# Optimization experiments

Measured on AMD Instinct MI355X. Metric: run time of the kernel, lower is better.

The kernel has to match this reference:

```python
import jax, jax.numpy as jnp
import numpy as np

HIDDEN_DIM = 256  # scale = sqrt(hidden_dim); D = 2*hidden_dim because is_bi_rnn=True
B, L, D = 4, 4096, 512


def setup_inputs() -> dict:
    key = jax.random.key(0)
    k1, k2, k3, k4, k5 = jax.random.split(key, 5)
    inputs = jax.random.normal(k1, (B, L, D), dtype=jnp.float32)
    # torch nn.Linear(D, D, bias=False) weights, applied as x @ W.T
    Wq = jax.random.normal(k2, (D, D), dtype=jnp.float32) / np.float32(np.sqrt(D))
    Wk = jax.random.normal(k3, (D, D), dtype=jnp.float32) / np.float32(np.sqrt(D))
    Wv = jax.random.normal(k4, (D, D), dtype=jnp.float32) / np.float32(np.sqrt(D))
    # valid lengths per batch element; max must equal L (source uses maxlen = max(lens))
    lens = jax.random.randint(k5, (B,), L // 2, L + 1).at[0].set(L)
    return {"inputs": inputs, "Wq": Wq, "Wk": Wk, "Wv": Wv, "lens": lens}


def reference(inputs, Wq, Wk, Wv, lens):
    # QKV projections (torch Linear: x @ W.T)
    Q = inputs @ Wq.T            # [B, L, D]
    K = inputs @ Wk.T            # [B, L, D]
    V = inputs @ Wv.T            # [B, L, D]
    scale = jnp.asarray(HIDDEN_DIM, inputs.dtype) ** 0.5
    scores = jnp.einsum('bqd,bkd->bqk', Q, K) / scale  # [B, L, L]
    # FAITHFUL: F.softmax with no dim on a 3-D tensor -> legacy torch dim=0 (batch axis)
    W = jax.nn.softmax(scores, axis=0)
    # post-softmax mask over QUERY rows: mask[b, q] = q < lens[b]
    mask = (jnp.arange(L)[None, :] < lens[:, None]).astype(W.dtype)  # [B, L]
    W = W * mask[:, :, None]
    Z = jnp.einsum('bqk,bkd->bqd', W, V)   # [B, L, D]
    return jnp.sum(Z, axis=1, keepdims=True)  # [B, 1, D]
```

## Files before the change

kernel.cpp:

```cpp
#include <hip/hip_runtime.h>

#define BB 4
#define LL 4096
#define DD 512

typedef __attribute__((ext_vector_type(8))) short bf16x8;
typedef __attribute__((ext_vector_type(4))) float f32x4;
typedef __attribute__((ext_vector_type(4))) unsigned short ushort4v;
typedef __attribute__((ext_vector_type(4))) unsigned int u32x4;

__device__ __forceinline__ unsigned short bf16_rne(float x) {
    unsigned u = __float_as_uint(x);
    unsigned r = (u + 0x7FFFu + ((u >> 16) & 1u)) >> 16;
    return (unsigned short)r;
}

__global__ __launch_bounds__(256) void split_x(const float* __restrict__ X,
                                               unsigned short* __restrict__ Xh,
                                               unsigned short* __restrict__ Xl) {
    const size_t i = ((size_t)blockIdx.x * 256 + threadIdx.x) * 4;
    float4 x4 = *reinterpret_cast<const float4*>(X + i);
    float v[4] = {x4.x, x4.y, x4.z, x4.w};
    ushort4v h4, l4;
    #pragma unroll
    for (int j = 0; j < 4; ++j) {
        unsigned short h = bf16_rne(v[j]);
        float lo = v[j] - __uint_as_float((unsigned)h << 16);
        h4[j] = h;
        l4[j] = bf16_rne(lo);
    }
    *reinterpret_cast<ushort4v*>(Xh + i) = h4;
    *reinterpret_cast<ushort4v*>(Xl + i) = l4;
}

__global__ __launch_bounds__(256) void gemm_tn_M(const float* __restrict__ A,
                                                 const float* __restrict__ B,
                                                 unsigned short* __restrict__ Mh,
                                                 unsigned short* __restrict__ Ml,
                                                 float scale) {
    __shared__ float As[16][68];
    __shared__ float Bs[16][68];
    const int tid = threadIdx.x;
    const int tx = tid & 15, ty = tid >> 4;
    const int iBase = blockIdx.x * 64;
    const int jBase = blockIdx.y * 64;
    const int dr = tid >> 4;
    const int c4 = (tid & 15) << 2;

    float acc[4][4] = {};
    for (int d0 = 0; d0 < DD; d0 += 16) {
        float4 a4 = *reinterpret_cast<const float4*>(A + (size_t)(d0 + dr) * DD + iBase + c4);
        float4 b4 = *reinterpret_cast<const float4*>(B + (size_t)(d0 + dr) * DD + jBase + c4);
        __syncthreads();
        *reinterpret_cast<float4*>(&As[dr][c4]) = a4;
        *reinterpret_cast<float4*>(&Bs[dr][c4]) = b4;
        __syncthreads();
        #pragma unroll
        for (int t = 0; t < 16; ++t) {
            float4 q4 = *reinterpret_cast<const float4*>(&As[t][ty << 2]);
            float4 k4 = *reinterpret_cast<const float4*>(&Bs[t][tx << 2]);
            float q[4] = {q4.x, q4.y, q4.z, q4.w};
            float k[4] = {k4.x, k4.y, k4.z, k4.w};
            #pragma unroll
            for (int i = 0; i < 4; ++i)
                #pragma unroll
                for (int j = 0; j < 4; ++j)
                    acc[i][j] = fmaf(q[i], k[j], acc[i][j]);
        }
    }
    #pragma unroll
    for (int i = 0; i < 4; ++i)
        #pragma unroll
        for (int j = 0; j < 4; ++j) {
            float v = acc[i][j] * scale;
            unsigned short h = bf16_rne(v);
            float lo = v - __uint_as_float((unsigned)h << 16);
            size_t off = (size_t)(iBase + (ty << 2) + i) * DD + jBase + (tx << 2) + j;
            Mh[off] = h;
            Ml[off] = bf16_rne(lo);
        }
}

#define GLOAD_LDS16(SRC, DST)                                                  \
    __builtin_amdgcn_global_load_lds(                                          \
        (const __attribute__((address_space(1))) void*)(SRC),                  \
        (__attribute__((address_space(3))) void*)(DST), 16, 0, 0)

__device__ __forceinline__ void stage8(const unsigned short* __restrict__ g,
                                       unsigned short* l) {
    const int ln = threadIdx.x & 63;
    const int r = ln >> 3;
    const int c = ln & 7;
    const unsigned short* src = g + (size_t)r * DD + ((c ^ r) << 3);
    GLOAD_LDS16(src, l);
}

__device__ __forceinline__ bf16x8 ldfrag(const unsigned short* base, int row16,
                                         int kk) {
    const int lane = threadIdx.x & 63;
    const int r = row16 + (lane & 15);
    const int boff = r * 128 + ((((kk + ((lane >> 4) << 3)) << 1)) ^ ((r & 7) << 4));
    return *reinterpret_cast<const bf16x8*>(
        reinterpret_cast<const char*>(base) + boff);
}

__global__ __launch_bounds__(256, 3) void gemm_nt_T(
    const unsigned short* __restrict__ Xh_g, const unsigned short* __restrict__ Xl_g,
    const unsigned short* __restrict__ Mh_g, const unsigned short* __restrict__ Ml_g,
    unsigned short* __restrict__ Th_g, unsigned short* __restrict__ Tl_g) {
    __shared__ unsigned short Ah_s[128][64];
    __shared__ unsigned short Al_s[128][64];
    __shared__ unsigned short Bh_s[64][64];
    __shared__ unsigned short Bl_s[64][64];

    const int lin = blockIdx.x;
    const int wgid = ((lin & 7) << 7) + (lin >> 3);
    const int rBase = (wgid >> 3) * 128;
    const int cBase = (wgid & 7) * 64;

    const int w = threadIdx.x >> 6;
    const int lane = threadIdx.x & 63;
    const int wq = (w >> 1) * 64;
    const int wk = (w & 1) * 32;

    f32x4 acc[4][2] = {};

    for (int dcc = 0; dcc < 8; ++dcc) {
        const int dc = dcc << 6;
        __syncthreads();
        #pragma unroll
        for (int s = 0; s < 4; ++s) {
            const int r0 = w * 32 + s * 8;
            stage8(Xh_g + (size_t)(rBase + r0) * DD + dc, &Ah_s[r0][0]);
            stage8(Xl_g + (size_t)(rBase + r0) * DD + dc, &Al_s[r0][0]);
        }
        #pragma unroll
        for (int s = 0; s < 2; ++s) {
            const int r0 = w * 16 + s * 8;
            stage8(Mh_g + (size_t)(cBase + r0) * DD + dc, &Bh_s[r0][0]);
            stage8(Ml_g + (size_t)(cBase + r0) * DD + dc, &Bl_s[r0][0]);
        }
        __syncthreads();
        #pragma unroll
        for (int kk = 0; kk < 64; kk += 32) {
            bf16x8 bh0 = ldfrag(&Bh_s[0][0], wk + 0, kk);
            bf16x8 bh1 = ldfrag(&Bh_s[0][0], wk + 16, kk);
            bf16x8 bl0 = ldfrag(&Bl_s[0][0], wk + 0, kk);
            bf16x8 bl1 = ldfrag(&Bl_s[0][0], wk + 16, kk);
            #pragma unroll
            for (int i = 0; i < 4; ++i) {
                bf16x8 ah = ldfrag(&Ah_s[0][0], wq + i * 16, kk);
                bf16x8 al = ldfrag(&Al_s[0][0], wq + i * 16, kk);
                acc[i][0] = __builtin_amdgcn_mfma_f32_16x16x32_bf16(ah, bh0, acc[i][0], 0, 0, 0);
                acc[i][0] = __builtin_amdgcn_mfma_f32_16x16x32_bf16(ah, bl0, acc[i][0], 0, 0, 0);
                acc[i][0] = __builtin_amdgcn_mfma_f32_16x16x32_bf16(al, bh0, acc[i][0], 0, 0, 0);
                acc[i][1] = __builtin_amdgcn_mfma_f32_16x16x32_bf16(ah, bh1, acc[i][1], 0, 0, 0);
                acc[i][1] = __builtin_amdgcn_mfma_f32_16x16x32_bf16(ah, bl1, acc[i][1], 0, 0, 0);
                acc[i][1] = __builtin_amdgcn_mfma_f32_16x16x32_bf16(al, bh1, acc[i][1], 0, 0, 0);
            }
        }
    }

    __syncthreads();
    char* hB = reinterpret_cast<char*>(&Ah_s[0][0]);
    char* lB = reinterpret_cast<char*>(&Al_s[0][0]);
    #pragma unroll
    for (int i = 0; i < 4; ++i)
        #pragma unroll
        for (int r = 0; r < 4; ++r) {
            const int row = wq + i * 16 + ((lane >> 4) << 2) + r;
            #pragma unroll
            for (int j = 0; j < 2; ++j) {
                const int col = wk + j * 16 + (lane & 15);
                float v = acc[i][j][r];
                unsigned short h = bf16_rne(v);
                float lo = v - __uint_as_float((unsigned)h << 16);
                const int bo = (row << 7) + (((col << 1)) ^ ((row & 7) << 4));
                *reinterpret_cast<unsigned short*>(hB + bo) = h;
                *reinterpret_cast<unsigned short*>(lB + bo) = bf16_rne(lo);
            }
        }
    __syncthreads();
    const int tid = threadIdx.x;
    #pragma unroll
    for (int s = 0; s < 4; ++s) {
        const int slot = s * 256 + tid;
        const int row = slot >> 3;
        const int sl = slot & 7;
        const int bo = (row << 7) + (((sl << 4)) ^ ((row & 7) << 4));
        u32x4 hv = *reinterpret_cast<const u32x4*>(hB + bo);
        u32x4 lv = *reinterpret_cast<const u32x4*>(lB + bo);
        const size_t go = (size_t)(rBase + row) * DD + cBase + (sl << 3);
        *reinterpret_cast<u32x4*>(Th_g + go) = hv;
        *reinterpret_cast<u32x4*>(Tl_g + go) = lv;
    }
}

__global__ __launch_bounds__(256, 3) void scores_wsum(
    const unsigned short* __restrict__ Qh_g, const unsigned short* __restrict__ Ql_g,
    const unsigned short* __restrict__ Kh_g, const unsigned short* __restrict__ Kl_g,
    const int* __restrict__ lens, float* __restrict__ wsum) {
    __shared__ unsigned short Qh_s[128][64];
    __shared__ unsigned short Ql_s[128][64];
    __shared__ unsigned short Kh_s[64][64];
    __shared__ unsigned short Kl_s[64][64];

    const int lin = blockIdx.x;
    const int wgid = ((lin & 7) << 8) + (lin >> 3);
    const int sub = wgid & 255;
    const int xcd = wgid >> 8;
    const int qBase = (((xcd & 1) << 4) + (sub & 15)) * 128;
    const int kBase = (((xcd >> 1) << 4) + (sub >> 4)) * 64;

    const int w = threadIdx.x >> 6;
    const int lane = threadIdx.x & 63;
    const int wq = (w >> 1) * 64;
    const int wk = (w & 1) * 32;

    const int l0 = lens[0], l1 = lens[1], l2 = lens[2], l3 = lens[3];

    f32x4 acc[4][4][2] = {};

    #pragma unroll
    for (int b = 0; b < BB; ++b) {
        const unsigned short* qh = Qh_g + (size_t)(b * LL + qBase) * DD;
        const unsigned short* ql = Ql_g + (size_t)(b * LL + qBase) * DD;
        const unsigned short* kh = Kh_g + (size_t)(b * LL + kBase) * DD;
        const unsigned short* kl = Kl_g + (size_t)(b * LL + kBase) * DD;
        for (int dcc = 0; dcc < 8; ++dcc) {
            const int dc = dcc << 6;
            __syncthreads();
            #pragma unroll
            for (int s = 0; s < 4; ++s) {
                const int r0 = w * 32 + s * 8;
                stage8(qh + (size_t)r0 * DD + dc, &Qh_s[r0][0]);
                stage8(ql + (size_t)r0 * DD + dc, &Ql_s[r0][0]);
            }
            #pragma unroll
            for (int s = 0; s < 2; ++s) {
                const int r0 = w * 16 + s * 8;
                stage8(kh + (size_t)r0 * DD + dc, &Kh_s[r0][0]);
                stage8(kl + (size_t)r0 * DD + dc, &Kl_s[r0][0]);
            }
            __syncthreads();
            #pragma unroll
            for (int kk = 0; kk < 64; kk += 32) {
                bf16x8 bh0 = ldfrag(&Kh_s[0][0], wk + 0, kk);
                bf16x8 bh1 = ldfrag(&Kh_s[0][0], wk + 16, kk);
                bf16x8 bl0 = ldfrag(&Kl_s[0][0], wk + 0, kk);
                bf16x8 bl1 = ldfrag(&Kl_s[0][0], wk + 16, kk);
                #pragma unroll
                for (int i = 0; i < 4; ++i) {
                    bf16x8 ah = ldfrag(&Qh_s[0][0], wq + i * 16, kk);
                    bf16x8 al = ldfrag(&Ql_s[0][0], wq + i * 16, kk);
                    acc[b][i][0] = __builtin_amdgcn_mfma_f32_16x16x32_bf16(ah, bh0, acc[b][i][0], 0, 0, 0);
                    acc[b][i][0] = __builtin_amdgcn_mfma_f32_16x16x32_bf16(ah, bl0, acc[b][i][0], 0, 0, 0);
                    acc[b][i][0] = __builtin_amdgcn_mfma_f32_16x16x32_bf16(al, bh0, acc[b][i][0], 0, 0, 0);
                    acc[b][i][1] = __builtin_amdgcn_mfma_f32_16x16x32_bf16(ah, bh1, acc[b][i][1], 0, 0, 0);
                    acc[b][i][1] = __builtin_amdgcn_mfma_f32_16x16x32_bf16(ah, bl1, acc[b][i][1], 0, 0, 0);
                    acc[b][i][1] = __builtin_amdgcn_mfma_f32_16x16x32_bf16(al, bh1, acc[b][i][1], 0, 0, 0);
                }
            }
        }
    }

    float psum[4][2] = {};
    #pragma unroll
    for (int i = 0; i < 4; ++i) {
        #pragma unroll
        for (int r = 0; r < 4; ++r) {
            const int q = qBase + wq + i * 16 + ((lane >> 4) << 2) + r;
            #pragma unroll
            for (int j = 0; j < 2; ++j) {
                float e0 = __expf(acc[0][i][j][r]);
                float e1 = __expf(acc[1][i][j][r]);
                float e2 = __expf(acc[2][i][j][r]);
                float e3 = __expf(acc[3][i][j][r]);
                float inv = 1.0f / (e0 + e1 + e2 + e3);
                psum[0][j] += (q < l0) ? e0 * inv : 0.0f;
                psum[1][j] += (q < l1) ? e1 * inv : 0.0f;
                psum[2][j] += (q < l2) ? e2 * inv : 0.0f;
                psum[3][j] += (q < l3) ? e3 * inv : 0.0f;
            }
        }
    }
    #pragma unroll
    for (int bb = 0; bb < 4; ++bb)
        #pragma unroll
        for (int j = 0; j < 2; ++j) {
            float v = psum[bb][j];
            v += __shfl_xor(v, 16);
            v += __shfl_xor(v, 32);
            if (lane < 16)
                atomicAdd(&wsum[bb * LL + kBase + wk + j * 16 + lane], v);
        }
}

__global__ __launch_bounds__(256) void wsum_x(const float* __restrict__ X,
                                              const float* __restrict__ wsum,
                                              float* __restrict__ y) {
    const int b = blockIdx.y;
    const int e = blockIdx.x * 256 + threadIdx.x;
    const int kc = blockIdx.z * 64;
    const float* Xp = X + ((size_t)b * LL + kc) * DD + e;
    const float* wp = wsum + b * LL + kc;
    float a = 0.0f;
    #pragma unroll 4
    for (int k = 0; k < 64; ++k) a = fmaf(wp[k], Xp[(size_t)k * DD], a);
    atomicAdd(&y[b * DD + e], a);
}

__global__ __launch_bounds__(256) void y_out(const float* __restrict__ Wv,
                                             const float* __restrict__ y,
                                             float* __restrict__ out) {
    const int b = blockIdx.y;
    const int d = blockIdx.x * 256 + threadIdx.x;
    const float* wv = Wv + (size_t)d * DD;
    const float* yb = y + b * DD;
    float a = 0.0f;
    #pragma unroll 4
    for (int e = 0; e < DD; e += 4) {
        float4 w4 = *reinterpret_cast<const float4*>(wv + e);
        float4 y4 = *reinterpret_cast<const float4*>(yb + e);
        a += w4.x * y4.x + w4.y * y4.y + w4.z * y4.z + w4.w * y4.w;
    }
    out[b * DD + d] = a;
}

extern "C" void kernel_launch(void* const* d_in, const int* in_sizes, int n_in,
                              void* d_out, int out_size, void* d_ws, size_t ws_size,
                              hipStream_t stream) {
    const float* X  = (const float*)d_in[0];
    const float* Wq = (const float*)d_in[1];
    const float* Wk = (const float*)d_in[2];
    const float* Wv = (const float*)d_in[3];
    const int* lens = (const int*)d_in[4];
    float* out = (float*)d_out;

    char* ws = (char*)d_ws;
    unsigned short* Xh  = (unsigned short*)ws;
    unsigned short* Xl  = (unsigned short*)(ws + ((size_t)16 << 20));
    unsigned short* Th  = (unsigned short*)(ws + ((size_t)32 << 20));
    unsigned short* Tl  = (unsigned short*)(ws + ((size_t)48 << 20));
    unsigned short* Mth = (unsigned short*)(ws + ((size_t)64 << 20));
    unsigned short* Mtl = (unsigned short*)(ws + ((size_t)64 << 20) + (512u << 10));
    float* wsum = (float*)(ws + ((size_t)65 << 20));
    float* y    = (float*)(ws + ((size_t)65 << 20) + 65536);

    hipMemsetAsync(wsum, 0,
                   (size_t)BB * LL * sizeof(float) + (size_t)BB * DD * sizeof(float),
                   stream);

    dim3 blk(256);
    split_x<<<dim3(8192), blk, 0, stream>>>(X, Xh, Xl);
    gemm_tn_M<<<dim3(8, 8), blk, 0, stream>>>(Wk, Wq, Mth, Mtl, 0.0625f);
    gemm_nt_T<<<dim3(1024), blk, 0, stream>>>(Xh, Xl, Mth, Mtl, Th, Tl);
    scores_wsum<<<dim3(2048), blk, 0, stream>>>(Th, Tl, Xh, Xl, lens, wsum);
    wsum_x<<<dim3(2, 4, 64), blk, 0, stream>>>(X, wsum, y);
    y_out<<<dim3(2, 4), blk, 0, stream>>>(Wv, y, out);
}
```

Before: 366.6 us.

## Double-buffer LDS tiles in scores_wsum and prefetch next chunk during MFMA

```diff
diff --git a/kernel.cpp b/kernel.cpp
--- a/kernel.cpp
+++ b/kernel.cpp
@@ -196,22 +196,17 @@
     }
 }
 
-__global__ __launch_bounds__(256, 3) void scores_wsum(
+__global__ __launch_bounds__(256) void scores_wsum(
     const unsigned short* __restrict__ Qh_g, const unsigned short* __restrict__ Ql_g,
     const unsigned short* __restrict__ Kh_g, const unsigned short* __restrict__ Kl_g,
     const int* __restrict__ lens, float* __restrict__ wsum) {
-    __shared__ unsigned short Qh_s[128][64];
-    __shared__ unsigned short Ql_s[128][64];
-    __shared__ unsigned short Kh_s[64][64];
-    __shared__ unsigned short Kl_s[64][64];
-
-    const int lin = blockIdx.x;
-    const int wgid = ((lin & 7) << 8) + (lin >> 3);
-    const int sub = wgid & 255;
-    const int xcd = wgid >> 8;
-    const int qBase = (((xcd & 1) << 4) + (sub & 15)) * 128;
-    const int kBase = (((xcd >> 1) << 4) + (sub >> 4)) * 64;
-
+    __shared__ unsigned short Qh_s[2][128][64];
+    __shared__ unsigned short Ql_s[2][128][64];
+    __shared__ unsigned short Kh_s[2][64][64];
+    __shared__ unsigned short Kl_s[2][64][64];
+
+    const int qBase = blockIdx.x * 128;
+    const int kBase = blockIdx.y * 64;
     const int w = threadIdx.x >> 6;
     const int lane = threadIdx.x & 63;
     const int wq = (w >> 1) * 64;
@@ -221,47 +216,92 @@
 
     f32x4 acc[4][4][2] = {};
 
-    #pragma unroll
-    for (int b = 0; b < BB; ++b) {
-        const unsigned short* qh = Qh_g + (size_t)(b * LL + qBase) * DD;
-        const unsigned short* ql = Ql_g + (size_t)(b * LL + qBase) * DD;
-        const unsigned short* kh = Kh_g + (size_t)(b * LL + kBase) * DD;
-        const unsigned short* kl = Kl_g + (size_t)(b * LL + kBase) * DD;
-        for (int dcc = 0; dcc < 8; ++dcc) {
-            const int dc = dcc << 6;
-            __syncthreads();
-            #pragma unroll
-            for (int s = 0; s < 4; ++s) {
-                const int r0 = w * 32 + s * 8;
-                stage8(qh + (size_t)r0 * DD + dc, &Qh_s[r0][0]);
-                stage8(ql + (size_t)r0 * DD + dc, &Ql_s[r0][0]);
+    auto stage = [&](int tn) {
+        const int bn = tn >> 3;
+        const int dcn = (tn & 7) << 6;
+        const int cb = tn & 1;
+        const unsigned short* qh = Qh_g + (size_t)(bn * LL + qBase) * DD + dcn;
+        const unsigned short* ql = Ql_g + (size_t)(bn * LL + qBase) * DD + dcn;
+        const unsigned short* kh = Kh_g + (size_t)(bn * LL + kBase) * DD + dcn;
+        const unsigned short* kl = Kl_g + (size_t)(bn * LL + kBase) * DD + dcn;
+        #pragma unroll
+        for (int s = 0; s < 4; ++s) {
+            const int r0 = w * 32 + s * 8;
+            stage8(qh + (size_t)r0 * DD, &Qh_s[cb][r0][0]);
+            stage8(ql + (size_t)r0 * DD, &Ql_s[cb][r0][0]);
+        }
+        #pragma unroll
+        for (int s = 0; s < 2; ++s) {
+            const int r0 = w * 16 + s * 8;
+            stage8(kh + (size_t)r0 * DD, &Kh_s[cb][r0][0]);
+            stage8(kl + (size_t)r0 * DD, &Kl_s[cb][r0][0]);
+        }
+    };
+
+    stage(0);
+
+    for (int t = 0; t < 32; ++t) {
+        if (t < 31) stage(t + 1);
+        if (t < 31)
+            asm volatile("s_waitcnt vmcnt(12)\n\ts_barrier" ::: "memory");
+        else
+            asm volatile("s_waitcnt vmcnt(0)\n\ts_barrier" ::: "memory");
+
+        const int cb = t & 1;
+        const int b = t >> 3;
+        const unsigned short* QhB = &Qh_s[cb][0][0];
+        const unsigned short* QlB = &Ql_s[cb][0][0];
+        const unsigned short* KhB = &Kh_s[cb][0][0];
+        const unsigned short* KlB = &Kl_s[cb][0][0];
+
+        f32x4 a0[4], a1[4];
+        #pragma unroll
+        for (int i = 0; i < 4; ++i) { a0[i] = acc[0][i][0]; a1[i] = acc[0][i][1]; }
+        if (b == 1) {
+            #pragma unroll
+            for (int i = 0; i < 4; ++i) { a0[i] = acc[1][i][0]; a1[i] = acc[1][i][1]; }
+        } else if (b == 2) {
+            #pragma unroll
+            for (int i = 0; i < 4; ++i) { a0[i] = acc[2][i][0]; a1[i] = acc[2][i][1]; }
+        } else if (b == 3) {
+            #pragma unroll
+            for (int i = 0; i < 4; ++i) { a0[i] = acc[3][i][0]; a1[i] = acc[3][i][1]; }
+        }
+
+        #pragma unroll
+        for (int kk = 0; kk < 64; kk += 32) {
+            bf16x8 bh0 = ldfrag(KhB, wk + 0, kk);
+            bf16x8 bh1 = ldfrag(KhB, wk + 16, kk);
+            bf16x8 bl0 = ldfrag(KlB, wk + 0, kk);
+            bf16x8 bl1 = ldfrag(KlB, wk + 16, kk);
+            #pragma unroll
+            for (int i = 0; i < 4; ++i) {
+                bf16x8 ah = ldfrag(QhB, wq + i * 16, kk);
+                bf16x8 al = ldfrag(QlB, wq + i * 16, kk);
+                a0[i] = __builtin_amdgcn_mfma_f32_16x16x32_bf16(ah, bh0, a0[i], 0, 0, 0);
+                a0[i] = __builtin_amdgcn_mfma_f32_16x16x32_bf16(ah, bl0, a0[i], 0, 0, 0);
+                a0[i] = __builtin_amdgcn_mfma_f32_16x16x32_bf16(al, bh0, a0[i], 0, 0, 0);
+                a1[i] = __builtin_amdgcn_mfma_f32_16x16x32_bf16(ah, bh1, a1[i], 0, 0, 0);
+                a1[i] = __builtin_amdgcn_mfma_f32_16x16x32_bf16(ah, bl1, a1[i], 0, 0, 0);
+                a1[i] = __builtin_amdgcn_mfma_f32_16x16x32_bf16(al, bh1, a1[i], 0, 0, 0);
             }
-            #pragma unroll
-            for (int s = 0; s < 2; ++s) {
-                const int r0 = w * 16 + s * 8;
-                stage8(kh + (size_t)r0 * DD + dc, &Kh_s[r0][0]);
-                stage8(kl + (size_t)r0 * DD + dc, &Kl_s[r0][0]);
-            }
-            __syncthreads();
-            #pragma unroll
-            for (int kk = 0; kk < 64; kk += 32) {
-                bf16x8 bh0 = ldfrag(&Kh_s[0][0], wk + 0, kk);
-                bf16x8 bh1 = ldfrag(&Kh_s[0][0], wk + 16, kk);
-                bf16x8 bl0 = ldfrag(&Kl_s[0][0], wk + 0, kk);
-                bf16x8 bl1 = ldfrag(&Kl_s[0][0], wk + 16, kk);
-                #pragma unroll
-                for (int i = 0; i < 4; ++i) {
-                    bf16x8 ah = ldfrag(&Qh_s[0][0], wq + i * 16, kk);
-                    bf16x8 al = ldfrag(&Ql_s[0][0], wq + i * 16, kk);
-                    acc[b][i][0] = __builtin_amdgcn_mfma_f32_16x16x32_bf16(ah, bh0, acc[b][i][0], 0, 0, 0);
-                    acc[b][i][0] = __builtin_amdgcn_mfma_f32_16x16x32_bf16(ah, bl0, acc[b][i][0], 0, 0, 0);
-                    acc[b][i][0] = __builtin_amdgcn_mfma_f32_16x16x32_bf16(al, bh0, acc[b][i][0], 0, 0, 0);
-                    acc[b][i][1] = __builtin_amdgcn_mfma_f32_16x16x32_bf16(ah, bh1, acc[b][i][1], 0, 0, 0);
-                    acc[b][i][1] = __builtin_amdgcn_mfma_f32_16x16x32_bf16(ah, bl1, acc[b][i][1], 0, 0, 0);
-                    acc[b][i][1] = __builtin_amdgcn_mfma_f32_16x16x32_bf16(al, bh1, acc[b][i][1], 0, 0, 0);
-                }
-            }
-        }
+        }
+
+        if (b == 0) {
+            #pragma unroll
+            for (int i = 0; i < 4; ++i) { acc[0][i][0] = a0[i]; acc[0][i][1] = a1[i]; }
+        } else if (b == 1) {
+            #pragma unroll
+            for (int i = 0; i < 4; ++i) { acc[1][i][0] = a0[i]; acc[1][i][1] = a1[i]; }
+        } else if (b == 2) {
+            #pragma unroll
+            for (int i = 0; i < 4; ++i) { acc[2][i][0] = a0[i]; acc[2][i][1] = a1[i]; }
+        } else {
+            #pragma unroll
+            for (int i = 0; i < 4; ++i) { acc[3][i][0] = a0[i]; acc[3][i][1] = a1[i]; }
+        }
+
+        asm volatile("s_barrier" ::: "memory");
     }
 
     float psum[4][2] = {};
@@ -355,7 +395,7 @@
     split_x<<<dim3(8192), blk, 0, stream>>>(X, Xh, Xl);
     gemm_tn_M<<<dim3(8, 8), blk, 0, stream>>>(Wk, Wq, Mth, Mtl, 0.0625f);
     gemm_nt_T<<<dim3(1024), blk, 0, stream>>>(Xh, Xl, Mth, Mtl, Th, Tl);
-    scores_wsum<<<dim3(2048), blk, 0, stream>>>(Th, Tl, Xh, Xl, lens, wsum);
+    scores_wsum<<<dim3(32, 64), blk, 0, stream>>>(Th, Tl, Xh, Xl, lens, wsum);
     wsum_x<<<dim3(2, 4, 64), blk, 0, stream>>>(X, wsum, y);
     y_out<<<dim3(2, 4), blk, 0, stream>>>(Wv, y, out);
 }
```

Result: slower. 594.5 us (+62.1%).
